# Kernel optimization log

Hardware: AMD Instinct MI355X
Metric: run time of the kernel (lower is better)

## Reference

```python
import jax, jax.numpy as jnp
import numpy as np

R, C, H, W = 500, 512, 38, 38      # rois, VGG channels, feature-map HxW (img 608 / 16)
K, HID, POOL, SCALE = 20, 4096, 3, 16
FEAT = C * POOL * POOL             # 4608, matches fc6 in_features


def setup_inputs():
    key = jax.random.key(0)
    ks = jax.random.split(key, 12)
    fmap = jax.random.normal(ks[0], (C, H, W), dtype=jnp.float32)
    # ROIs in original image coords (x1,y1,x2,y2); width/height >= 48 px so that
    # after /16 + floor every ROI is non-degenerate (none filtered out).
    x1 = jax.random.randint(ks[1], (R,), 0, 288)
    y1 = jax.random.randint(ks[2], (R,), 0, 288)
    bw = jax.random.randint(ks[3], (R,), 48, 304)
    bh = jax.random.randint(ks[4], (R,), 48, 304)
    rois = jnp.stack([x1, y1, x1 + bw, y1 + bh], axis=1).astype(jnp.float32)
    label = jax.random.bernoulli(ks[5], 0.3, (K,)).astype(jnp.float32)
    s = 0.01
    W6 = jax.random.normal(ks[6], (FEAT, HID), jnp.float32) * s
    b6 = jnp.zeros((HID,), jnp.float32)
    W7 = jax.random.normal(ks[7], (HID, HID), jnp.float32) * s
    b7 = jnp.zeros((HID,), jnp.float32)
    W8c = jax.random.normal(ks[8], (HID, K), jnp.float32) * s
    b8c = jnp.zeros((K,), jnp.float32)
    W8d = jax.random.normal(ks[9], (HID, K), jnp.float32) * s
    b8d = jnp.zeros((K,), jnp.float32)
    return dict(fmap=fmap, rois=rois, label=label, W6=W6, b6=b6, W7=W7, b7=b7,
                W8c=W8c, b8c=b8c, W8d=W8d, b8d=b8d)


def _roi_pool(fmap, rois):
    # scaled_rois = origin_rois / 16, sliced as integer indices (floor)
    sc = jnp.floor(rois / SCALE).astype(jnp.int32)          # [R,4]
    x1, y1, x2, y2 = sc[:, 0], sc[:, 1], sc[:, 2], sc[:, 3]

    def binmask(lo, hi, size):
        # adaptive-max-pool bins: [lo + floor(j*L/3), lo + ceil((j+1)*L/3))
        L = hi - lo                                          # [R]
        j = jnp.arange(POOL)
        start = lo[:, None] + (j[None, :] * L[:, None]) // POOL
        end = lo[:, None] + (-((-(j[None, :] + 1) * L[:, None]) // POOL))
        pos = jnp.arange(size)
        return (pos[None, None, :] >= start[:, :, None]) & (pos[None, None, :] < end[:, :, None])

    cm = binmask(x1, x2, W)                                  # [R,3,W]
    rm = binmask(y1, y2, H)                                  # [R,3,H]
    neg = jnp.finfo(fmap.dtype).min
    # max over x within each x-bin: [R,C,H,3]
    tmp = jnp.max(jnp.where(cm[:, None, None, :, :], fmap[None, :, :, None, :], neg), axis=-1)
    # max over y within each y-bin: [R,C,3,3]
    pooled = jnp.max(jnp.where(rm[:, None, :, :, None], tmp[:, :, None, :, :], neg), axis=3)
    return pooled.reshape(R, FEAT), sc.astype(jnp.float32)


def _spatial_reg(scores, fc7, rois_sc, label):
    # faithful to original: argsort ascending, index 0 taken as the reference box,
    # and bboxes_iou interprets (x1,y1,x2,y2) as (x,y,w,h) — replicated as-is.
    idx = jnp.argsort(scores, axis=0)                        # [R,K]

    def per_class(idx_k, s_k, lab_k):
        h, rest = idx_k[0], idx_k[1:]
        hb = rois_sc[h]                                      # [4]
        rb = rois_sc[rest]                                   # [R-1,4]
        b1x2, b1y2 = rb[:, 0] + rb[:, 2], rb[:, 1] + rb[:, 3]
        b2x2, b2y2 = hb[0] + hb[2], hb[1] + hb[3]
        iw = jnp.clip(jnp.minimum(b1x2, b2x2) - jnp.maximum(rb[:, 0], hb[0]) + 1, 0)
        ih = jnp.clip(jnp.minimum(b1y2, b2y2) - jnp.maximum(rb[:, 1], hb[1]) + 1, 0)
        inter = iw * ih
        a1 = (b1x2 - rb[:, 0] + 1) * (b1y2 - rb[:, 1] + 1)
        a2 = (b2x2 - hb[0] + 1) * (b2y2 - hb[1] + 1)
        iou = inter / (a1 + a2 - inter)
        m = (iou > 0.6).astype(fc7.dtype)                    # [R-1]
        rf = fc7[rest] * m[:, None]
        diff = (rf - fc7[h]) * s_k[rest][:, None]
        return lab_k * 0.5 * jnp.sum(diff * diff)

    regs = jax.vmap(per_class)(idx.T, scores.T, label)       # [K]
    return jnp.sum(regs) / K


def reference(fmap, rois, label, W6, b6, W7, b7, W8c, b8c, W8d, b8d):
    feat, rois_sc = _roi_pool(fmap, rois)                    # [R,4608]
    fc6 = feat @ W6 + b6
    fc7 = fc6 @ W7 + b7
    pc = jax.nn.softmax(fc7 @ W8c + b8c, axis=1)             # per-roi over classes
    pd = jax.nn.softmax(fc7 @ W8d + b8d, axis=0)             # per-class over rois
    scores = pc * pd                                         # [R,K]
    out = jnp.sum(scores, axis=0)                            # [K], in (0,1)
    bce = -jnp.mean(label * jnp.log(out) + (1.0 - label) * jnp.log(1.0 - out))
    reg = _spatial_reg(scores, fc7, rois_sc, label)
    return scores, bce + reg, reg
```

## Files before the change

kernel.cpp:

```cpp
#include <hip/hip_runtime.h>
#include <cstdint>
#include <cstddef>

#define DEV __device__ __forceinline__

typedef __bf16 bf16_t;
typedef __bf16 bf16x8 __attribute__((ext_vector_type(8)));
typedef float  f32x4  __attribute__((ext_vector_type(4)));
typedef unsigned int u32x4 __attribute__((ext_vector_type(4)));

DEV bf16_t f2bf(float x) { return (bf16_t)x; }

constexpr int R_ = 500, C_ = 512, H_ = 38, W_ = 38, K_ = 20;
constexpr int HID = 4096, FEAT = 4608, MP = 512;
constexpr int HW = H_ * W_;

constexpr size_t alup(size_t x) { return (x + 255) & ~(size_t)255; }
constexpr size_t O_FMT  = 0;
constexpr size_t O_RSC  = alup(O_FMT  + (size_t)HW*C_*4);
constexpr size_t O_FEAT = alup(O_RSC  + (size_t)R_*4*4);
constexpr size_t O_FC6  = alup(O_FEAT + (size_t)MP*FEAT*2);
constexpr size_t O_FC7  = alup(O_FC6  + (size_t)MP*HID*2);
constexpr size_t O_PC   = alup(O_FC7  + (size_t)MP*HID*4);
constexpr size_t O_LD   = alup(O_PC   + (size_t)R_*K_*4);
constexpr size_t O_AN   = alup(O_LD   + (size_t)R_*K_*4);
constexpr size_t O_OS   = alup(O_AN   + (size_t)MP*4);
constexpr size_t O_HI   = alup(O_OS   + (size_t)K_*4);
constexpr size_t O_D    = alup(O_HI   + (size_t)K_*4);
constexpr size_t O_W8T  = alup(O_D    + (size_t)R_*K_*4);
constexpr size_t O_PART = alup(O_W8T  + (size_t)2*K_*HID*4);
constexpr size_t WS_K4  = O_PART + (size_t)4*MP*HID*4;

__global__ void __launch_bounds__(256) k_transpose(const float* __restrict__ fmap,
                                                   float* __restrict__ fmapt) {
    __shared__ float tile[32][33];
    int p0 = blockIdx.x * 32, c0 = blockIdx.y * 32;
    int tx = threadIdx.x & 31, ty = threadIdx.x >> 5;
#pragma unroll
    for (int i = 0; i < 4; ++i) {
        int c = c0 + ty + i*8, p = p0 + tx;
        tile[ty + i*8][tx] = (p < HW) ? fmap[(size_t)c*HW + p] : 0.f;
    }
    __syncthreads();
#pragma unroll
    for (int i = 0; i < 4; ++i) {
        int p = p0 + ty + i*8, c = c0 + tx;
        if (p < HW) fmapt[(size_t)p*C_ + c] = tile[tx][ty + i*8];
    }
}

__global__ void __launch_bounds__(256) k_w8t(const float* __restrict__ W8c,
                                             const float* __restrict__ W8d,
                                             float* __restrict__ W8T) {
    int k = blockIdx.x;
    const float* src = (k < K_) ? W8c : W8d;
    int kk = (k < K_) ? k : k - K_;
    for (int i = threadIdx.x; i < HID; i += 256)
        W8T[(size_t)k*HID + i] = src[(size_t)i*K_ + kk];
}

__global__ void __launch_bounds__(256) k_roipool(const float* __restrict__ fmapt,
                                                 const float* __restrict__ rois,
                                                 bf16_t* __restrict__ feat,
                                                 float* __restrict__ rois_sc) {
    int r = blockIdx.x, bin = blockIdx.y, t = threadIdx.x;
    if (r >= R_) {
        feat[(size_t)r*FEAT + (size_t)t*9       + bin] = (bf16_t)0.f;
        feat[(size_t)r*FEAT + (size_t)(t+256)*9 + bin] = (bf16_t)0.f;
        return;
    }
    int x1 = (int)floorf(rois[r*4+0] * 0.0625f);
    int y1 = (int)floorf(rois[r*4+1] * 0.0625f);
    int x2 = (int)floorf(rois[r*4+2] * 0.0625f);
    int y2 = (int)floorf(rois[r*4+3] * 0.0625f);
    if (bin == 0 && t == 0) {
        rois_sc[r*4+0] = (float)x1; rois_sc[r*4+1] = (float)y1;
        rois_sc[r*4+2] = (float)x2; rois_sc[r*4+3] = (float)y2;
    }
    int Lx = x2 - x1, Ly = y2 - y1;
    int pr = bin / 3, px = bin - pr*3;
    int rs = y1 + (pr*Ly)/3, re = y1 + ((pr+1)*Ly + 2)/3;
    int cs = x1 + (px*Lx)/3, ce = x1 + ((px+1)*Lx + 2)/3;
    float m0 = -3.402823466e38f, m1 = -3.402823466e38f;
    for (int y = rs; y < re; ++y) {
        const float* rowp = fmapt + (size_t)(y*W_)*C_;
        for (int x = cs; x < ce; ++x) {
            const float* p = rowp + (size_t)x*C_;
            m0 = fmaxf(m0, p[t]);
            m1 = fmaxf(m1, p[t + 256]);
        }
    }
    feat[(size_t)r*FEAT + (size_t)t*9       + bin] = f2bf(m0);
    feat[(size_t)r*FEAT + (size_t)(t+256)*9 + bin] = f2bf(m1);
}

__global__ void __launch_bounds__(256, 2)
k_gemm(const bf16_t* __restrict__ A, const float* __restrict__ B,
       float* __restrict__ part, int KDIM, int nts) {
    __shared__ bf16_t Al[2][128][72];
    __shared__ bf16_t Bl[2][128][72];
    const int t = threadIdx.x;
    const int lane = t & 63, wid = t >> 6;
    const int wr = wid >> 1, wc = wid & 1;

    const int flat = blockIdx.x + 32 * (blockIdx.y + 4 * blockIdx.z);
    const int xcd = flat & 7, slot = flat >> 3;
    const int grp = xcd * 16 + (slot >> 2);
    const int by = slot & 3;
    const int bx = grp & 31, bz = grp >> 5;

    const int brow = by * 128, bcol = bx * 128;
    const int kt0 = bz * nts;

    f32x4 acc[4][4] = {};
    u32x4 areg[4];
    float breg[4][8];

    auto load_tile = [&](int kt) {
        const int k0 = kt * 64;
#pragma unroll
        for (int i = 0; i < 4; ++i) {
            int slot2 = t + i*256;
            int row = slot2 >> 3, kg = slot2 & 7;
            areg[i] = *reinterpret_cast<const u32x4*>(A + (size_t)(brow + row)*KDIM + k0 + kg*8);
        }
#pragma unroll
        for (int i = 0; i < 4; ++i) {
            int slot2 = t + i*256;
            int n = slot2 & 127, kg = slot2 >> 7;
            const float* src = B + (size_t)(k0 + kg*8)*HID + bcol + n;
#pragma unroll
            for (int j = 0; j < 8; ++j) breg[i][j] = src[(size_t)j*HID];
        }
    };
    auto write_tile = [&](int buf) {
#pragma unroll
        for (int i = 0; i < 4; ++i) {
            int slot2 = t + i*256;
            int row = slot2 >> 3, kg = slot2 & 7;
            *reinterpret_cast<u32x4*>(&Al[buf][row][kg*8]) = areg[i];
        }
#pragma unroll
        for (int i = 0; i < 4; ++i) {
            int slot2 = t + i*256;
            int n = slot2 & 127, kg = slot2 >> 7;
            bf16x8 v;
#pragma unroll
            for (int j = 0; j < 8; ++j) v[j] = f2bf(breg[i][j]);
            *reinterpret_cast<bf16x8*>(&Bl[buf][n][kg*8]) = v;
        }
    };

    load_tile(kt0);
    write_tile(0);
    __syncthreads();

    for (int it = 0; it < nts; ++it) {
        const int cur = it & 1;
        if (it + 1 < nts) load_tile(kt0 + it + 1);
#pragma unroll
        for (int kk = 0; kk < 2; ++kk) {
            bf16x8 af[4], bfr[4];
#pragma unroll
            for (int m = 0; m < 4; ++m)
                af[m] = *reinterpret_cast<const bf16x8*>(
                    &Al[cur][wr*64 + m*16 + (lane & 15)][kk*32 + (lane >> 4)*8]);
#pragma unroll
            for (int n = 0; n < 4; ++n)
                bfr[n] = *reinterpret_cast<const bf16x8*>(
                    &Bl[cur][wc*64 + n*16 + (lane & 15)][kk*32 + (lane >> 4)*8]);
#pragma unroll
            for (int m = 0; m < 4; ++m)
#pragma unroll
                for (int n = 0; n < 4; ++n)
                    acc[m][n] = __builtin_amdgcn_mfma_f32_16x16x32_bf16(af[m], bfr[n], acc[m][n], 0, 0, 0);
        }
        if (it + 1 < nts) { write_tile(cur ^ 1); __syncthreads(); }
    }

    float* dst = part + (size_t)bz * MP * HID;
#pragma unroll
    for (int m = 0; m < 4; ++m) {
        int row0 = brow + wr*64 + m*16 + ((lane >> 4) << 2);
#pragma unroll
        for (int n = 0; n < 4; ++n) {
            int col = bcol + wc*64 + n*16 + (lane & 15);
#pragma unroll
            for (int j = 0; j < 4; ++j)
                dst[(size_t)(row0 + j)*HID + col] = acc[m][n][j];
        }
    }
}

__global__ void __launch_bounds__(256) k_reduce(const float* __restrict__ part,
                                                const float* __restrict__ bias,
                                                bf16_t* __restrict__ ob, float* __restrict__ of,
                                                int ksplit) {
    size_t idx = ((size_t)blockIdx.x*256 + threadIdx.x) * 4;
    f32x4 s = *reinterpret_cast<const f32x4*>(part + idx);
    for (int ss = 1; ss < ksplit; ++ss)
        s += *reinterpret_cast<const f32x4*>(part + (size_t)ss*MP*HID + idx);
    int col = (int)(idx & (HID - 1));
    s += *reinterpret_cast<const f32x4*>(bias + col);
    if (ob) {
#pragma unroll
        for (int j = 0; j < 4; ++j) ob[idx + j] = f2bf(s[j]);
    } else {
        *reinterpret_cast<f32x4*>(of + idx) = s;
    }
}

__global__ void __launch_bounds__(256) k_heads(const float* __restrict__ fc7,
        const float* __restrict__ W8T,
        const float* __restrict__ b8c, const float* __restrict__ b8d,
        float* __restrict__ pc, float* __restrict__ ld_out, float* __restrict__ An) {
    int r = blockIdx.x, t = threadIdx.x;
    float ac[20] = {}, ad[20] = {}, aa = 0.f;
    const float* frow = fc7 + (size_t)r*HID;
    for (int e = 0; e < 16; ++e) {
        int i = e*256 + t;
        float x = frow[i];
        aa = fmaf(x, x, aa);
#pragma unroll
        for (int k = 0; k < 20; ++k) {
            ac[k] = fmaf(x, W8T[(size_t)k*HID + i], ac[k]);
            ad[k] = fmaf(x, W8T[(size_t)(K_ + k)*HID + i], ad[k]);
        }
    }
#pragma unroll
    for (int k = 0; k < 20; ++k)
        for (int off = 1; off < 64; off <<= 1) {
            ac[k] += __shfl_xor(ac[k], off, 64);
            ad[k] += __shfl_xor(ad[k], off, 64);
        }
    for (int off = 1; off < 64; off <<= 1) aa += __shfl_xor(aa, off, 64);

    __shared__ float red[4][41];
    int wid = t >> 6, lane = t & 63;
    if (lane == 0) {
#pragma unroll
        for (int k = 0; k < 20; ++k) { red[wid][k] = ac[k]; red[wid][20+k] = ad[k]; }
        red[wid][40] = aa;
    }
    __syncthreads();
    __shared__ float lcs[20];
    if (t < 41) {
        float v = red[0][t] + red[1][t] + red[2][t] + red[3][t];
        if (t < 20)      lcs[t] = v + b8c[t];
        else if (t < 40) ld_out[r*K_ + (t-20)] = v + b8d[t-20];
        else             An[r] = v;
    }
    __syncthreads();
    if (t == 0) {
        float mx = lcs[0];
#pragma unroll
        for (int k = 1; k < 20; ++k) mx = fmaxf(mx, lcs[k]);
        float s = 0.f, e[20];
#pragma unroll
        for (int k = 0; k < 20; ++k) { e[k] = expf(lcs[k] - mx); s += e[k]; }
        float inv = 1.f / s;
#pragma unroll
        for (int k = 0; k < 20; ++k) pc[r*K_ + k] = e[k] * inv;
    }
}

__global__ void __launch_bounds__(256) k_pd(const float* __restrict__ ld,
        const float* __restrict__ pc, float* __restrict__ scores,
        float* __restrict__ out_sum, int* __restrict__ h_idx) {
    int k = blockIdx.x, t = threadIdx.x;
    __shared__ float sh[4];
    float m = -3.402823466e38f;
    for (int r = t; r < R_; r += 256) m = fmaxf(m, ld[r*K_ + k]);
    for (int off = 1; off < 64; off <<= 1) m = fmaxf(m, __shfl_xor(m, off, 64));
    if ((t & 63) == 0) sh[t >> 6] = m;
    __syncthreads();
    m = fmaxf(fmaxf(sh[0], sh[1]), fmaxf(sh[2], sh[3]));
    __syncthreads();
    float s = 0.f;
    for (int r = t; r < R_; r += 256) s += expf(ld[r*K_ + k] - m);
    for (int off = 1; off < 64; off <<= 1) s += __shfl_xor(s, off, 64);
    if ((t & 63) == 0) sh[t >> 6] = s;
    __syncthreads();
    s = sh[0] + sh[1] + sh[2] + sh[3];
    float inv = 1.f / s;

    float osum = 0.f, bv = 3.402823466e38f; int bi = 0x7fffffff;
    for (int r = t; r < R_; r += 256) {
        float p  = expf(ld[r*K_ + k] - m) * inv;
        float sc = pc[r*K_ + k] * p;
        scores[r*K_ + k] = sc;
        osum += sc;
        if (sc < bv || (sc == bv && r < bi)) { bv = sc; bi = r; }
    }
    for (int off = 1; off < 64; off <<= 1) osum += __shfl_xor(osum, off, 64);
    for (int off = 1; off < 64; off <<= 1) {
        float v2 = __shfl_xor(bv, off, 64);
        int   i2 = __shfl_xor(bi, off, 64);
        if (v2 < bv || (v2 == bv && i2 < bi)) { bv = v2; bi = i2; }
    }
    __shared__ float so[4], mv[4]; __shared__ int mi[4];
    if ((t & 63) == 0) { so[t >> 6] = osum; mv[t >> 6] = bv; mi[t >> 6] = bi; }
    __syncthreads();
    if (t == 0) {
        out_sum[k] = so[0] + so[1] + so[2] + so[3];
        float v = mv[0]; int i = mi[0];
        for (int w = 1; w < 4; ++w)
            if (mv[w] < v || (mv[w] == v && mi[w] < i)) { v = mv[w]; i = mi[w]; }
        h_idx[k] = i;
    }
}

__global__ void __launch_bounds__(256) k_dmat(const float* __restrict__ fc7,
        const int* __restrict__ h_idx, float* __restrict__ D) {
    int r = blockIdx.x, t = threadIdx.x;
    const float* frow = fc7 + (size_t)r*HID;
    const float* hrow[20];
#pragma unroll
    for (int k = 0; k < 20; ++k) hrow[k] = fc7 + (size_t)h_idx[k]*HID;
    float acc[20] = {};
    for (int e = 0; e < 16; ++e) {
        int i = e*256 + t;
        float x = frow[i];
#pragma unroll
        for (int k = 0; k < 20; ++k) acc[k] = fmaf(x, hrow[k][i], acc[k]);
    }
#pragma unroll
    for (int k = 0; k < 20; ++k)
        for (int off = 1; off < 64; off <<= 1) acc[k] += __shfl_xor(acc[k], off, 64);
    __shared__ float red[4][20];
    int wid = t >> 6, lane = t & 63;
    if (lane == 0) {
#pragma unroll
        for (int k = 0; k < 20; ++k) red[wid][k] = acc[k];
    }
    __syncthreads();
    if (t < 20) D[r*K_ + t] = red[0][t] + red[1][t] + red[2][t] + red[3][t];
}

__global__ void __launch_bounds__(256) k_final(const float* __restrict__ out_sum,
        const int* __restrict__ h_idx, const float* __restrict__ label,
        const float* __restrict__ scores, const float* __restrict__ D,
        const float* __restrict__ An, const float* __restrict__ rois_sc,
        float* __restrict__ dout) {
    int t = threadIdx.x;
    __shared__ float bsh[20];
    if (t < 20) {
        float o = out_sum[t], lab = label[t];
        bsh[t] = lab * logf(o) + (1.f - lab) * logf(1.f - o);
    }
    __syncthreads();

    float rp = 0.f;
    for (int i = t; i < R_*K_; i += 256) {
        int r = i / 20, k = i - r*20;
        int h = h_idx[k];
        if (r == h) continue;
        float lab = label[k];
        if (lab == 0.f) continue;
        float s = scores[r*K_ + k];
        const float* rb = rois_sc + r*4;
        const float* hb = rois_sc + h*4;
        float b1x2 = rb[0] + rb[2], b1y2 = rb[1] + rb[3];
        float b2x2 = hb[0] + hb[2], b2y2 = hb[1] + hb[3];
        float iw = fmaxf(fminf(b1x2, b2x2) - fmaxf(rb[0], hb[0]) + 1.f, 0.f);
        float ih = fmaxf(fminf(b1y2, b2y2) - fmaxf(rb[1], hb[1]) + 1.f, 0.f);
        float inter = iw * ih;
        float a1 = (b1x2 - rb[0] + 1.f) * (b1y2 - rb[1] + 1.f);
        float a2 = (b2x2 - hb[0] + 1.f) * (b2y2 - hb[1] + 1.f);
        float iou = inter / (a1 + a2 - inter);
        float mm = (iou > 0.6f) ? 1.f : 0.f;
        float term = mm * (An[r] - 2.f * D[r*K_ + k]) + An[h];
        rp += lab * 0.5f * s * s * term;
    }
    for (int off = 1; off < 64; off <<= 1) rp += __shfl_xor(rp, off, 64);
    __shared__ float rsh[4];
    if ((t & 63) == 0) rsh[t >> 6] = rp;
    __syncthreads();
    if (t == 0) {
        float reg = (rsh[0] + rsh[1] + rsh[2] + rsh[3]) / (float)K_;
        float b = 0.f;
        for (int k = 0; k < 20; ++k) b += bsh[k];
        float bce = -b / (float)K_;
        dout[R_*K_]     = bce + reg;
        dout[R_*K_ + 1] = reg;
    }
}

extern "C" void kernel_launch(void* const* d_in, const int* in_sizes, int n_in,
                              void* d_out, int out_size, void* d_ws, size_t ws_size,
                              hipStream_t stream) {
    const float* fmap  = (const float*)d_in[0];
    const float* rois  = (const float*)d_in[1];
    const float* label = (const float*)d_in[2];
    const float* W6    = (const float*)d_in[3];
    const float* b6    = (const float*)d_in[4];
    const float* W7    = (const float*)d_in[5];
    const float* b7    = (const float*)d_in[6];
    const float* W8c   = (const float*)d_in[7];
    const float* b8c   = (const float*)d_in[8];
    const float* W8d   = (const float*)d_in[9];
    const float* b8d   = (const float*)d_in[10];
    char* ws = (char*)d_ws;
    float* out = (float*)d_out;

    float*  fmapt = (float*)(ws + O_FMT);
    float*  roisc = (float*)(ws + O_RSC);
    bf16_t* feat  = (bf16_t*)(ws + O_FEAT);
    bf16_t* fc6   = (bf16_t*)(ws + O_FC6);
    float*  fc7   = (float*)(ws + O_FC7);
    float*  pc    = (float*)(ws + O_PC);
    float*  ld    = (float*)(ws + O_LD);
    float*  An    = (float*)(ws + O_AN);
    float*  osum  = (float*)(ws + O_OS);
    int*    hidx  = (int*)(ws + O_HI);
    float*  Dm    = (float*)(ws + O_D);
    float*  w8t   = (float*)(ws + O_W8T);
    float*  part  = (float*)(ws + O_PART);

    int ksplit = (ws_size >= WS_K4) ? 4 : 1;

    k_transpose<<<dim3((HW + 31)/32, C_/32), dim3(256), 0, stream>>>(fmap, fmapt);
    k_w8t      <<<dim3(2*K_),   dim3(256), 0, stream>>>(W8c, W8d, w8t);
    k_roipool  <<<dim3(MP, 9),  dim3(256), 0, stream>>>(fmapt, rois, feat, roisc);

    k_gemm  <<<dim3(HID/128, MP/128, ksplit), dim3(256), 0, stream>>>(feat, W6, part, FEAT, (FEAT/64)/ksplit);
    k_reduce<<<dim3((MP*HID)/1024), dim3(256), 0, stream>>>(part, b6, fc6, (float*)nullptr, ksplit);

    k_gemm  <<<dim3(HID/128, MP/128, ksplit), dim3(256), 0, stream>>>(fc6, W7, part, HID, (HID/64)/ksplit);
    k_reduce<<<dim3((MP*HID)/1024), dim3(256), 0, stream>>>(part, b7, (bf16_t*)nullptr, fc7, ksplit);

    k_heads<<<dim3(R_), dim3(256), 0, stream>>>(fc7, w8t, b8c, b8d, pc, ld, An);
    k_pd   <<<dim3(K_), dim3(256), 0, stream>>>(ld, pc, out, osum, hidx);
    k_dmat <<<dim3(R_), dim3(256), 0, stream>>>(fc7, hidx, Dm);
    k_final<<<dim3(1),  dim3(256), 0, stream>>>(osum, hidx, label, out, Dm, An, roisc, out);
}
```

Measured before the change: 176.6 us.

## Shrink GEMM N-tile to 64, swizzle LDS, single-buffer, raise occupancy

The FC GEMM tile drops from 128x128 to 128x64, and the grid grows to 64x4x4 blocks with a new XCD-aware block mapping. The padded double-buffered LDS is replaced by one XOR-swizzled buffer, and W tiles are loaded as float2 vectors. Launch bounds go to 4 blocks per SM so that latency is hidden by occupancy rather than double buffering. The price is an extra barrier per k-step, less reuse of each A tile, and ksplit hardcoded to 4 whether or not the workspace is large enough.

```diff
diff --git a/kernel.cpp b/kernel.cpp
--- a/kernel.cpp
+++ b/kernel.cpp
@@ -7,6 +7,7 @@
 typedef __bf16 bf16_t;
 typedef __bf16 bf16x8 __attribute__((ext_vector_type(8)));
 typedef float  f32x4  __attribute__((ext_vector_type(4)));
+typedef float  f32x2  __attribute__((ext_vector_type(2)));
 typedef unsigned int u32x4 __attribute__((ext_vector_type(4)));
 
 DEV bf16_t f2bf(float x) { return (bf16_t)x; }
@@ -94,88 +95,87 @@
     feat[(size_t)r*FEAT + (size_t)(t+256)*9 + bin] = f2bf(m1);
 }
 
-__global__ void __launch_bounds__(256, 2)
+__global__ void __launch_bounds__(256, 4)
 k_gemm(const bf16_t* __restrict__ A, const float* __restrict__ B,
        float* __restrict__ part, int KDIM, int nts) {
-    __shared__ bf16_t Al[2][128][72];
-    __shared__ bf16_t Bl[2][128][72];
+    __shared__ bf16_t Asm[128*64];
+    __shared__ bf16_t Bsm[64*64];
     const int t = threadIdx.x;
     const int lane = t & 63, wid = t >> 6;
     const int wr = wid >> 1, wc = wid & 1;
 
-    const int flat = blockIdx.x + 32 * (blockIdx.y + 4 * blockIdx.z);
-    const int xcd = flat & 7, slot = flat >> 3;
-    const int grp = xcd * 16 + (slot >> 2);
-    const int by = slot & 3;
-    const int bx = grp & 31, bz = grp >> 5;
-
-    const int brow = by * 128, bcol = bx * 128;
+    const int flat = blockIdx.x + 64*blockIdx.y + 256*blockIdx.z;
+    const int v = (flat & 7)*128 + (flat >> 3);
+    const int by = v & 3, bx = (v >> 2) & 63, bz = v >> 8;
+
+    const int brow = by * 128, bcol = bx * 64;
     const int kt0 = bz * nts;
 
-    f32x4 acc[4][4] = {};
+    f32x4 acc[4][2] = {};
     u32x4 areg[4];
-    float breg[4][8];
-
-    auto load_tile = [&](int kt) {
+    f32x2 br[8];
+
+    const int n2 = t & 31, kgl = t >> 5;
+
+    auto load_regs = [&](int kt) {
         const int k0 = kt * 64;
 #pragma unroll
         for (int i = 0; i < 4; ++i) {
-            int slot2 = t + i*256;
-            int row = slot2 >> 3, kg = slot2 & 7;
+            int s = t + i*256;
+            int row = s >> 3, kg = s & 7;
             areg[i] = *reinterpret_cast<const u32x4*>(A + (size_t)(brow + row)*KDIM + k0 + kg*8);
         }
+        const float* srcB = B + (size_t)(k0 + kgl*8)*HID + bcol + n2*2;
+#pragma unroll
+        for (int j = 0; j < 8; ++j)
+            br[j] = *reinterpret_cast<const f32x2*>(srcB + (size_t)j*HID);
+    };
+    auto write_lds = [&]() {
 #pragma unroll
         for (int i = 0; i < 4; ++i) {
-            int slot2 = t + i*256;
-            int n = slot2 & 127, kg = slot2 >> 7;
-            const float* src = B + (size_t)(k0 + kg*8)*HID + bcol + n;
-#pragma unroll
-            for (int j = 0; j < 8; ++j) breg[i][j] = src[(size_t)j*HID];
-        }
+            int s = t + i*256;
+            int row = s >> 3, kg = s & 7;
+            int pos = row*8 + (kg ^ ((row >> 1) & 7));
+            *reinterpret_cast<u32x4*>(Asm + pos*8) = areg[i];
+        }
+        bf16x8 v0, v1;
+#pragma unroll
+        for (int j = 0; j < 8; ++j) { v0[j] = f2bf(br[j].x); v1[j] = f2bf(br[j].y); }
+        int kbsw = kgl ^ (n2 & 7);
+        *reinterpret_cast<u32x4*>(Bsm + ((2*n2    )*8 + kbsw)*8) = *reinterpret_cast<u32x4*>(&v0);
+        *reinterpret_cast<u32x4*>(Bsm + ((2*n2 + 1)*8 + kbsw)*8) = *reinterpret_cast<u32x4*>(&v1);
     };
-    auto write_tile = [&](int buf) {
-#pragma unroll
-        for (int i = 0; i < 4; ++i) {
-            int slot2 = t + i*256;
-            int row = slot2 >> 3, kg = slot2 & 7;
-            *reinterpret_cast<u32x4*>(&Al[buf][row][kg*8]) = areg[i];
-        }
-#pragma unroll
-        for (int i = 0; i < 4; ++i) {
-            int slot2 = t + i*256;
-            int n = slot2 & 127, kg = slot2 >> 7;
-            bf16x8 v;
-#pragma unroll
-            for (int j = 0; j < 8; ++j) v[j] = f2bf(breg[i][j]);
-            *reinterpret_cast<bf16x8*>(&Bl[buf][n][kg*8]) = v;
-        }
-    };
-
-    load_tile(kt0);
-    write_tile(0);
+
+    load_regs(kt0);
+    write_lds();
     __syncthreads();
 
     for (int it = 0; it < nts; ++it) {
-        const int cur = it & 1;
-        if (it + 1 < nts) load_tile(kt0 + it + 1);
+        if (it + 1 < nts) load_regs(kt0 + it + 1);
 #pragma unroll
         for (int kk = 0; kk < 2; ++kk) {
-            bf16x8 af[4], bfr[4];
+            const int kb = kk*4 + (lane >> 4);
+            bf16x8 af[4], bfr[2];
+#pragma unroll
+            for (int m = 0; m < 4; ++m) {
+                int row = wr*64 + m*16 + (lane & 15);
+                af[m] = *reinterpret_cast<const bf16x8*>(
+                    Asm + (row*8 + (kb ^ ((row >> 1) & 7)))*8);
+            }
+#pragma unroll
+            for (int n = 0; n < 2; ++n) {
+                int nn = wc*32 + n*16 + (lane & 15);
+                bfr[n] = *reinterpret_cast<const bf16x8*>(
+                    Bsm + (nn*8 + (kb ^ ((nn >> 1) & 7)))*8);
+            }
 #pragma unroll
             for (int m = 0; m < 4; ++m)
-                af[m] = *reinterpret_cast<const bf16x8*>(
-                    &Al[cur][wr*64 + m*16 + (lane & 15)][kk*32 + (lane >> 4)*8]);
-#pragma unroll
-            for (int n = 0; n < 4; ++n)
-                bfr[n] = *reinterpret_cast<const bf16x8*>(
-                    &Bl[cur][wc*64 + n*16 + (lane & 15)][kk*32 + (lane >> 4)*8]);
-#pragma unroll
-            for (int m = 0; m < 4; ++m)
-#pragma unroll
-                for (int n = 0; n < 4; ++n)
+#pragma unroll
+                for (int n = 0; n < 2; ++n)
                     acc[m][n] = __builtin_amdgcn_mfma_f32_16x16x32_bf16(af[m], bfr[n], acc[m][n], 0, 0, 0);
         }
-        if (it + 1 < nts) { write_tile(cur ^ 1); __syncthreads(); }
+        __syncthreads();
+        if (it + 1 < nts) { write_lds(); __syncthreads(); }
     }
 
     float* dst = part + (size_t)bz * MP * HID;
@@ -183,8 +183,8 @@
     for (int m = 0; m < 4; ++m) {
         int row0 = brow + wr*64 + m*16 + ((lane >> 4) << 2);
 #pragma unroll
-        for (int n = 0; n < 4; ++n) {
-            int col = bcol + wc*64 + n*16 + (lane & 15);
+        for (int n = 0; n < 2; ++n) {
+            int col = bcol + wc*32 + n*16 + (lane & 15);
 #pragma unroll
             for (int j = 0; j < 4; ++j)
                 dst[(size_t)(row0 + j)*HID + col] = acc[m][n][j];
@@ -417,16 +417,16 @@
     float*  w8t   = (float*)(ws + O_W8T);
     float*  part  = (float*)(ws + O_PART);
 
-    int ksplit = (ws_size >= WS_K4) ? 4 : 1;
+    const int ksplit = 4;
 
     k_transpose<<<dim3((HW + 31)/32, C_/32), dim3(256), 0, stream>>>(fmap, fmapt);
     k_w8t      <<<dim3(2*K_),   dim3(256), 0, stream>>>(W8c, W8d, w8t);
     k_roipool  <<<dim3(MP, 9),  dim3(256), 0, stream>>>(fmapt, rois, feat, roisc);
 
-    k_gemm  <<<dim3(HID/128, MP/128, ksplit), dim3(256), 0, stream>>>(feat, W6, part, FEAT, (FEAT/64)/ksplit);
+    k_gemm  <<<dim3(HID/64, MP/128, ksplit), dim3(256), 0, stream>>>(feat, W6, part, FEAT, (FEAT/64)/ksplit);
     k_reduce<<<dim3((MP*HID)/1024), dim3(256), 0, stream>>>(part, b6, fc6, (float*)nullptr, ksplit);
 
-    k_gemm  <<<dim3(HID/128, MP/128, ksplit), dim3(256), 0, stream>>>(fc6, W7, part, HID, (HID/64)/ksplit);
+    k_gemm  <<<dim3(HID/64, MP/128, ksplit), dim3(256), 0, stream>>>(fc6, W7, part, HID, (HID/64)/ksplit);
     k_reduce<<<dim3((MP*HID)/1024), dim3(256), 0, stream>>>(part, b7, (bf16_t*)nullptr, fc7, ksplit);
 
     k_heads<<<dim3(R_), dim3(256), 0, stream>>>(fc7, w8t, b8c, b8d, pc, ld, An);
```

Measured after the change: 184.2 us. 1.04x slower.

## Stage GEMM A tiles directly into swizzled LDS and vectorize B loads

Applied to the files above, without the earlier changes.

The GEMM kernel now copies A tiles from global memory straight into LDS with global_load_lds, using an XOR-swizzled layout. This replaces the register round-trip and the padded array. B is loaded as float2 pairs, converted to bf16 and written into a matching swizzled LDS layout. Block-index remapping is generalized and the K-split is hard-coded to 4, dropping the workspace-size check. The aim is fewer load instructions, fewer LDS bank conflicts and less register staging. The risk is correctness around completion of the asynchronous LDS loads and the assumption that the workspace is always large enough.

```diff
diff --git a/kernel.cpp b/kernel.cpp
--- a/kernel.cpp
+++ b/kernel.cpp
@@ -7,6 +7,7 @@
 typedef __bf16 bf16_t;
 typedef __bf16 bf16x8 __attribute__((ext_vector_type(8)));
 typedef float  f32x4  __attribute__((ext_vector_type(4)));
+typedef float  f32x2  __attribute__((ext_vector_type(2)));
 typedef unsigned int u32x4 __attribute__((ext_vector_type(4)));
 
 DEV bf16_t f2bf(float x) { return (bf16_t)x; }
@@ -97,85 +98,88 @@
 __global__ void __launch_bounds__(256, 2)
 k_gemm(const bf16_t* __restrict__ A, const float* __restrict__ B,
        float* __restrict__ part, int KDIM, int nts) {
-    __shared__ bf16_t Al[2][128][72];
-    __shared__ bf16_t Bl[2][128][72];
+    __shared__ bf16_t Asm[2][128*64];
+    __shared__ bf16_t Bsm[2][128*64];
     const int t = threadIdx.x;
     const int lane = t & 63, wid = t >> 6;
     const int wr = wid >> 1, wc = wid & 1;
 
-    const int flat = blockIdx.x + 32 * (blockIdx.y + 4 * blockIdx.z);
-    const int xcd = flat & 7, slot = flat >> 3;
-    const int grp = xcd * 16 + (slot >> 2);
-    const int by = slot & 3;
-    const int bx = grp & 31, bz = grp >> 5;
+    const int flat = blockIdx.x + 32*blockIdx.y + 128*blockIdx.z;
+    const int q = 16 * gridDim.z;
+    const int v = (flat & 7) * q + (flat >> 3);
+    const int by = v & 3, bx = (v >> 2) & 31, bz = v >> 7;
 
     const int brow = by * 128, bcol = bx * 128;
     const int kt0 = bz * nts;
 
     f32x4 acc[4][4] = {};
-    u32x4 areg[4];
-    float breg[4][8];
-
-    auto load_tile = [&](int kt) {
-        const int k0 = kt * 64;
+    f32x2 br[16];
+    const int n2 = t & 63, kgl = t >> 6;
+
+    auto stage_A = [&](int kt, int buf) {
+        const bf16_t* Ag = A + (size_t)brow*KDIM + kt*64;
 #pragma unroll
         for (int i = 0; i < 4; ++i) {
-            int slot2 = t + i*256;
-            int row = slot2 >> 3, kg = slot2 & 7;
-            areg[i] = *reinterpret_cast<const u32x4*>(A + (size_t)(brow + row)*KDIM + k0 + kg*8);
-        }
-#pragma unroll
-        for (int i = 0; i < 4; ++i) {
-            int slot2 = t + i*256;
-            int n = slot2 & 127, kg = slot2 >> 7;
-            const float* src = B + (size_t)(k0 + kg*8)*HID + bcol + n;
-#pragma unroll
-            for (int j = 0; j < 8; ++j) breg[i][j] = src[(size_t)j*HID];
+            int s = t + i*256;
+            int row = s >> 3;
+            int kb = (s & 7) ^ ((row >> 1) & 7);
+            const bf16_t* src = Ag + (size_t)row*KDIM + kb*8;
+            bf16_t* dst = &Asm[buf][(size_t)(i*256 + (t & ~63)) * 8];
+            __builtin_amdgcn_global_load_lds(
+                (const __attribute__((address_space(1))) void*)src,
+                (__attribute__((address_space(3))) void*)dst, 16, 0, 0);
         }
     };
-    auto write_tile = [&](int buf) {
-#pragma unroll
-        for (int i = 0; i < 4; ++i) {
-            int slot2 = t + i*256;
-            int row = slot2 >> 3, kg = slot2 & 7;
-            *reinterpret_cast<u32x4*>(&Al[buf][row][kg*8]) = areg[i];
-        }
-#pragma unroll
-        for (int i = 0; i < 4; ++i) {
-            int slot2 = t + i*256;
-            int n = slot2 & 127, kg = slot2 >> 7;
-            bf16x8 v;
-#pragma unroll
-            for (int j = 0; j < 8; ++j) v[j] = f2bf(breg[i][j]);
-            *reinterpret_cast<bf16x8*>(&Bl[buf][n][kg*8]) = v;
-        }
+    auto load_B = [&](int kt) {
+        const float* src = B + (size_t)(kt*64 + kgl*16)*HID + bcol + 2*n2;
+#pragma unroll
+        for (int j = 0; j < 16; ++j)
+            br[j] = *reinterpret_cast<const f32x2*>(src + (size_t)j*HID);
     };
-
-    load_tile(kt0);
-    write_tile(0);
+    auto write_B = [&](int buf) {
+        const int sw = n2 & 7;
+        bf16x8 v0, v1;
+#pragma unroll
+        for (int j = 0; j < 8; ++j) { v0[j] = f2bf(br[j].x); v1[j] = f2bf(br[j+8].x); }
+        *reinterpret_cast<u32x4*>(&Bsm[buf][(size_t)((2*n2)*8 + ((kgl*2    ) ^ sw)) * 8]) = *reinterpret_cast<u32x4*>(&v0);
+        *reinterpret_cast<u32x4*>(&Bsm[buf][(size_t)((2*n2)*8 + ((kgl*2 + 1) ^ sw)) * 8]) = *reinterpret_cast<u32x4*>(&v1);
+#pragma unroll
+        for (int j = 0; j < 8; ++j) { v0[j] = f2bf(br[j].y); v1[j] = f2bf(br[j+8].y); }
+        *reinterpret_cast<u32x4*>(&Bsm[buf][(size_t)((2*n2+1)*8 + ((kgl*2    ) ^ sw)) * 8]) = *reinterpret_cast<u32x4*>(&v0);
+        *reinterpret_cast<u32x4*>(&Bsm[buf][(size_t)((2*n2+1)*8 + ((kgl*2 + 1) ^ sw)) * 8]) = *reinterpret_cast<u32x4*>(&v1);
+    };
+
+    stage_A(kt0, 0);
+    load_B(kt0);
+    write_B(0);
     __syncthreads();
 
     for (int it = 0; it < nts; ++it) {
         const int cur = it & 1;
-        if (it + 1 < nts) load_tile(kt0 + it + 1);
+        if (it + 1 < nts) { stage_A(kt0 + it + 1, cur ^ 1); load_B(kt0 + it + 1); }
 #pragma unroll
         for (int kk = 0; kk < 2; ++kk) {
+            const int kb = kk*4 + (lane >> 4);
             bf16x8 af[4], bfr[4];
 #pragma unroll
-            for (int m = 0; m < 4; ++m)
+            for (int m = 0; m < 4; ++m) {
+                int row = wr*64 + m*16 + (lane & 15);
                 af[m] = *reinterpret_cast<const bf16x8*>(
-                    &Al[cur][wr*64 + m*16 + (lane & 15)][kk*32 + (lane >> 4)*8]);
-#pragma unroll
-            for (int n = 0; n < 4; ++n)
+                    &Asm[cur][(size_t)(row*8 + (kb ^ ((row >> 1) & 7))) * 8]);
+            }
+#pragma unroll
+            for (int n = 0; n < 4; ++n) {
+                int nn = wc*64 + n*16 + (lane & 15);
                 bfr[n] = *reinterpret_cast<const bf16x8*>(
-                    &Bl[cur][wc*64 + n*16 + (lane & 15)][kk*32 + (lane >> 4)*8]);
+                    &Bsm[cur][(size_t)(nn*8 + (kb ^ ((nn >> 1) & 7))) * 8]);
+            }
 #pragma unroll
             for (int m = 0; m < 4; ++m)
 #pragma unroll
                 for (int n = 0; n < 4; ++n)
                     acc[m][n] = __builtin_amdgcn_mfma_f32_16x16x32_bf16(af[m], bfr[n], acc[m][n], 0, 0, 0);
         }
-        if (it + 1 < nts) { write_tile(cur ^ 1); __syncthreads(); }
+        if (it + 1 < nts) { write_B(cur ^ 1); __syncthreads(); }
     }
 
     float* dst = part + (size_t)bz * MP * HID;
@@ -417,7 +421,7 @@
     float*  w8t   = (float*)(ws + O_W8T);
     float*  part  = (float*)(ws + O_PART);
 
-    int ksplit = (ws_size >= WS_K4) ? 4 : 1;
+    const int ksplit = 4;
 
     k_transpose<<<dim3((HW + 31)/32, C_/32), dim3(256), 0, stream>>>(fmap, fmapt);
     k_w8t      <<<dim3(2*K_),   dim3(256), 0, stream>>>(W8c, W8d, w8t);
```

After: 180.5 us. 1.02x slower.
